# Optimization experiments

Measured on AMD Instinct MI355X. Metric: run time of the kernel, lower is better.

The kernel has to match this reference:

```python
import jax, jax.numpy as jnp
import numpy as np

B, SRC_SEQ, SRC_DIMS = 1024, 336, 64
ORDER, TAR_SEQ = 168, 96


def setup_inputs() -> dict:
    key = jax.random.key(0)
    k1, k2 = jax.random.split(key, 2)
    inputs = jax.random.normal(k1, (B, SRC_SEQ, SRC_DIMS), dtype=jnp.float32)
    # Per-channel Dense(order -> tar_seq_len): stacked kernels and biases.
    W = jax.random.normal(k2, (SRC_DIMS, ORDER, TAR_SEQ), dtype=jnp.float32) * (1.0 / np.sqrt(ORDER))
    b = jnp.zeros((SRC_DIMS, TAR_SEQ), dtype=jnp.float32)
    return {"inputs": inputs, "W": W, "b": b, "training": 0}


def reference(inputs, W, b, training):
    # inputs: [B, S, C]; W: [C, order, T]; b: [C, T]
    order = W.shape[1]
    x = jnp.transpose(inputs, (0, 2, 1))[:, :, -order:]  # [B, C, order]
    # Fused per-channel linear projection (batched over channels):
    y = jnp.einsum('bco,cot->bct', x, W) + b             # [B, C, T]
    return jnp.transpose(y, (0, 2, 1))                    # [B, T, C]
```

## Files before the change

kernel.cpp:

```cpp
#include <hip/hip_runtime.h>

#define BATCH 1024
#define SEQ   336
#define CCH   64
#define ORD   168
#define TT    96
#define OFF   168
#define KP    192
#define RSC   25
#define YSTR  12

typedef __attribute__((ext_vector_type(8))) short  short8;
typedef __attribute__((ext_vector_type(8))) unsigned short ushort8;
typedef __attribute__((ext_vector_type(4))) float  floatx4;

#define WT2_ELEMS ((size_t)CCH * 36 * 512)
#define WS_NEED   (WT2_ELEMS * 2)
#define K2_LDS    (8 * 32 * RSC * 16)

__device__ __forceinline__ unsigned short f2bf(float f) {
    union { float f; unsigned u; } v; v.f = f;
    unsigned r = v.u + 0x7FFF + ((v.u >> 16) & 1);
    return (unsigned short)(r >> 16);
}

__global__ __launch_bounds__(256)
void k1w(const float* __restrict__ W, unsigned short* __restrict__ Wt2)
{
    const int tid = threadIdx.x, l = tid & 63, w = tid >> 6;
    const int wid = blockIdx.x * 4 + w;
    const int kc = wid % 6;
    const int n  = (wid / 6) % 6;
    const int c  = wid / 36;
    const int m  = l & 15, kg = l >> 4;
    const int t  = n * 16 + m;
    ushort8 u;
    #pragma unroll
    for (int j = 0; j < 8; ++j) {
        int o = kc * 32 + kg * 8 + j;
        float val = (o < ORD) ? W[((size_t)c * ORD + o) * TT + t] : 0.f;
        u[j] = f2bf(val);
    }
    *(ushort8*)(Wt2 + (size_t)wid * 512 + l * 8) = u;
}

__global__ __launch_bounds__(512, 2)
void k2f(const float* __restrict__ inp, const unsigned short* __restrict__ Wt2,
         const float* __restrict__ bias, float* __restrict__ out)
{
    extern __shared__ float smem_f[];
    unsigned short* Xs = (unsigned short*)smem_f;

    const int tid = threadIdx.x, l = tid & 63, wv = tid >> 6;
    const int m = l & 15, kg = l >> 4;
    const int btile = (blockIdx.x & 7) | ((blockIdx.x >> 6) << 3);
    const int cg    = (blockIdx.x >> 3) & 7;
    const int b0 = btile * 32, c0 = cg * 8;

    #pragma unroll
    for (int i = 0; i < 3; ++i) {
        int v = tid + i * 512;
        int cq = v & 1, b = (v >> 1) & 31, kchunk = v >> 6;
        floatx4 f[8];
        #pragma unroll
        for (int j = 0; j < 8; ++j) {
            int o = kchunk * 8 + j;
            floatx4 z = {0.f, 0.f, 0.f, 0.f};
            f[j] = (o < ORD)
                ? *(const floatx4*)(inp + ((size_t)(b0 + b) * SEQ + OFF + o) * CCH + c0 + cq * 4)
                : z;
        }
        #pragma unroll
        for (int cc = 0; cc < 4; ++cc) {
            int c = cq * 4 + cc;
            ushort8 u;
            #pragma unroll
            for (int j = 0; j < 8; ++j) u[j] = f2bf(f[j][cc]);
            *(ushort8*)(Xs + (((c * 32 + b) * RSC + (kchunk ^ (c & 7))) << 3)) = u;
        }
    }

    float bv[6];
    #pragma unroll
    for (int n = 0; n < 6; ++n)
        bv[n] = bias[(c0 + wv) * TT + n * 16 + m];

    __syncthreads();

    floatx4 acc0[6] = {}, acc1[6] = {};
    {
        const unsigned short* Wc = Wt2 + (size_t)(c0 + wv) * 36 * 512;
        #pragma unroll
        for (int kc = 0; kc < 6; ++kc) {
            int chunk = (kc * 4 + kg) ^ (wv & 7);
            short8 a0 = *(const short8*)(Xs + (((wv * 32 + m)      * RSC + chunk) << 3));
            short8 a1 = *(const short8*)(Xs + (((wv * 32 + 16 + m) * RSC + chunk) << 3));
            #pragma unroll
            for (int n = 0; n < 6; ++n) {
                short8 bfrag = *(const short8*)(Wc + (size_t)(n * 6 + kc) * 512 + l * 8);
                acc0[n] = __builtin_amdgcn_mfma_f32_16x16x32_bf16(a0, bfrag, acc0[n], 0, 0, 0);
                acc1[n] = __builtin_amdgcn_mfma_f32_16x16x32_bf16(a1, bfrag, acc1[n], 0, 0, 0);
            }
        }
    }

    __syncthreads();

    float* Ys = smem_f;
    #pragma unroll
    for (int rnd = 0; rnd < 2; ++rnd) {
        {
            #pragma unroll
            for (int n = 0; n < 6; ++n)
                #pragma unroll
                for (int r = 0; r < 4; ++r) {
                    int row = kg * 4 + r;
                    float val = (rnd == 0 ? acc0[n][r] : acc1[n][r]) + bv[n];
                    Ys[(row * TT + n * 16 + m) * YSTR + wv] = val;
                }
        }
        __syncthreads();
        {
            int c4  = tid & 1;
            int te  = (tid >> 1) & 15;
            int row = tid >> 5;
            #pragma unroll
            for (int s = 0; s < 6; ++s) {
                int tt = te + s * 16;
                floatx4 y = *(const floatx4*)(Ys + (row * TT + tt) * YSTR + c4 * 4);
                *(floatx4*)(out + ((size_t)(b0 + rnd * 16 + row) * TT + tt) * CCH + c0 + c4 * 4) = y;
            }
        }
        __syncthreads();
    }
}

#define MB  8
#define NT  16
#define KO  8
#define NCH (ORD/KO)
#define WSTRIDE 132
typedef __attribute__((address_space(3))) void* lds_ptr_t;
typedef const __attribute__((address_space(1))) void* gbl_ptr_t;

__global__ __launch_bounds__(256, 4)
void tcl_fallback(const float* __restrict__ inp, const float* __restrict__ W,
                  const float* __restrict__ bias, float* __restrict__ out)
{
    __shared__ float Xsf[MB * KO * CCH];
    __shared__ float Wsf[CCH * WSTRIDE];
    const int tid = threadIdx.x;
    const int c   = tid & 63;
    const int tg  = tid >> 6;
    const int bblk = blockIdx.x & 127;
    const int tblk = blockIdx.x >> 7;
    const int b0 = bblk * MB;
    const int t0 = tblk * NT;
    float acc[MB][4];
    #pragma unroll
    for (int bi = 0; bi < MB; ++bi)
        #pragma unroll
        for (int tj = 0; tj < 4; ++tj) acc[bi][tj] = 0.f;
    for (int ch = 0; ch < NCH; ++ch) {
        const int ob = ch * KO;
        #pragma unroll
        for (int k = 0; k < 4; ++k) {
            int v = tid + k * 256;
            int row = v >> 4, c4 = v & 15;
            int bi = row >> 3, oi = row & 7;
            const float* gp = inp + ((size_t)(b0 + bi) * SEQ + (OFF + ob + oi)) * CCH + c4 * 4;
            __builtin_amdgcn_global_load_lds((gbl_ptr_t)gp, (lds_ptr_t)(Xsf + v * 4), 16, 0, 0);
        }
        float4 wbuf[8];
        #pragma unroll
        for (int k = 0; k < 8; ++k) {
            int v = tid + k * 256;
            int cch = v >> 5, oi = (v >> 2) & 7, t4 = v & 3;
            wbuf[k] = *(const float4*)(W + (size_t)cch * (ORD * TT) + (size_t)(ob + oi) * TT + t0 + t4 * 4);
        }
        #pragma unroll
        for (int k = 0; k < 8; ++k) {
            int v = tid + k * 256;
            int cch = v >> 5, oi = (v >> 2) & 7, t4 = v & 3;
            *(float4*)(Wsf + cch * WSTRIDE + oi * NT + t4 * 4) = wbuf[k];
        }
        __syncthreads();
        #pragma unroll
        for (int oi = 0; oi < KO; ++oi) {
            const float4 wvv = *(const float4*)(Wsf + c * WSTRIDE + oi * NT + tg * 4);
            float xv[MB];
            #pragma unroll
            for (int bi = 0; bi < MB; ++bi) xv[bi] = Xsf[(bi * KO + oi) * CCH + c];
            #pragma unroll
            for (int bi = 0; bi < MB; ++bi) {
                acc[bi][0] += xv[bi] * wvv.x;
                acc[bi][1] += xv[bi] * wvv.y;
                acc[bi][2] += xv[bi] * wvv.z;
                acc[bi][3] += xv[bi] * wvv.w;
            }
        }
        __syncthreads();
    }
    const float4 bvv = *(const float4*)(bias + c * TT + t0 + tg * 4);
    #pragma unroll
    for (int bi = 0; bi < MB; ++bi) {
        size_t base = ((size_t)(b0 + bi) * TT + (t0 + tg * 4)) * CCH + c;
        out[base]           = acc[bi][0] + bvv.x;
        out[base + CCH]     = acc[bi][1] + bvv.y;
        out[base + 2 * CCH] = acc[bi][2] + bvv.z;
        out[base + 3 * CCH] = acc[bi][3] + bvv.w;
    }
}

extern "C" void kernel_launch(void* const* d_in, const int* in_sizes, int n_in,
                              void* d_out, int out_size, void* d_ws, size_t ws_size,
                              hipStream_t stream) {
    const float* inp  = (const float*)d_in[0];
    const float* W    = (const float*)d_in[1];
    const float* bias = (const float*)d_in[2];
    float* out = (float*)d_out;

    if (ws_size >= WS_NEED) {
        unsigned short* Wt2 = (unsigned short*)d_ws;
        k1w<<<576, 256, 0, stream>>>(W, Wt2);
        k2f<<<256, 512, K2_LDS, stream>>>(inp, Wt2, bias, out);
    } else {
        tcl_fallback<<<768, 256, 0, stream>>>(inp, W, bias, out);
    }
}
```

Before: 147.3 us.

## Switch to 32x32x16 MFMA with register-resident weights and smaller channel tiles

Rewrites the main GEMM kernel to use 32x32x16 bf16 MFMA instead of 16x16x32. Each wave now preloads its channel's full weight fragments (36 short8) into registers, and the weight-packing layout changes to match. Blocks shrink to 256 threads covering 4 channels x 32 batches, and the grid doubles to 512 blocks. This cuts LDS weight traffic and instruction count and gives more blocks, but raises register pressure and makes the output store only 16 bytes wide per row.

Result: slower. 157.3 us (+6.8%).

```diff
diff --git a/kernel.cpp b/kernel.cpp
--- a/kernel.cpp
+++ b/kernel.cpp
@@ -7,16 +7,14 @@
 #define TT    96
 #define OFF   168
 #define KP    192
-#define RSC   25
-#define YSTR  12
-
-typedef __attribute__((ext_vector_type(8))) short  short8;
-typedef __attribute__((ext_vector_type(8))) unsigned short ushort8;
-typedef __attribute__((ext_vector_type(4))) float  floatx4;
-
-#define WT2_ELEMS ((size_t)CCH * 36 * 512)
-#define WS_NEED   (WT2_ELEMS * 2)
-#define K2_LDS    (8 * 32 * RSC * 16)
+
+typedef __attribute__((ext_vector_type(8)))  short  short8;
+typedef __attribute__((ext_vector_type(8)))  unsigned short ushort8;
+typedef __attribute__((ext_vector_type(4)))  float  floatx4;
+typedef __attribute__((ext_vector_type(16))) float  floatx16;
+
+#define WT3_ELEMS ((size_t)CCH * 36 * 512)
+#define WS_NEED   (WT3_ELEMS * 2)
 
 __device__ __forceinline__ unsigned short f2bf(float f) {
     union { float f; unsigned u; } v; v.f = f;
@@ -25,113 +23,105 @@
 }
 
 __global__ __launch_bounds__(256)
-void k1w(const float* __restrict__ W, unsigned short* __restrict__ Wt2)
+void k1w(const float* __restrict__ W, unsigned short* __restrict__ Wt3)
 {
     const int tid = threadIdx.x, l = tid & 63, w = tid >> 6;
     const int wid = blockIdx.x * 4 + w;
-    const int kc = wid % 6;
-    const int n  = (wid / 6) % 6;
+    const int kt = wid % 12;
+    const int n  = (wid / 12) % 3;
     const int c  = wid / 36;
-    const int m  = l & 15, kg = l >> 4;
-    const int t  = n * 16 + m;
+    const int tm = l & 31, kh = l >> 5;
+    const int t  = n * 32 + tm;
     ushort8 u;
     #pragma unroll
     for (int j = 0; j < 8; ++j) {
-        int o = kc * 32 + kg * 8 + j;
+        int o = kt * 16 + kh * 8 + j;
         float val = (o < ORD) ? W[((size_t)c * ORD + o) * TT + t] : 0.f;
         u[j] = f2bf(val);
     }
-    *(ushort8*)(Wt2 + (size_t)wid * 512 + l * 8) = u;
-}
-
-__global__ __launch_bounds__(512, 2)
-void k2f(const float* __restrict__ inp, const unsigned short* __restrict__ Wt2,
+    *(ushort8*)(Wt3 + (size_t)wid * 512 + l * 8) = u;
+}
+
+__global__ __launch_bounds__(256, 2)
+void k2g(const float* __restrict__ inp, const unsigned short* __restrict__ Wt3,
          const float* __restrict__ bias, float* __restrict__ out)
 {
-    extern __shared__ float smem_f[];
-    unsigned short* Xs = (unsigned short*)smem_f;
+    __shared__ unsigned short XsU[4 * 12 * 64 * 8];
 
     const int tid = threadIdx.x, l = tid & 63, wv = tid >> 6;
-    const int m = l & 15, kg = l >> 4;
-    const int btile = (blockIdx.x & 7) | ((blockIdx.x >> 6) << 3);
-    const int cg    = (blockIdx.x >> 3) & 7;
-    const int b0 = btile * 32, c0 = cg * 8;
-
-    #pragma unroll
-    for (int i = 0; i < 3; ++i) {
-        int v = tid + i * 512;
-        int cq = v & 1, b = (v >> 1) & 31, kchunk = v >> 6;
+    const int tm = l & 31;
+    const int btile = (blockIdx.x & 7) | ((blockIdx.x >> 7) << 3);
+    const int cg    = (blockIdx.x >> 3) & 15;
+    const int b0 = btile * 32, c0 = cg * 4;
+
+    const unsigned short* Wc = Wt3 + (size_t)(c0 + wv) * 36 * 512 + l * 8;
+    short8 bfr[36];
+    #pragma unroll
+    for (int q = 0; q < 36; ++q)
+        bfr[q] = *(const short8*)(Wc + (size_t)q * 512);
+
+    float bv[3];
+    #pragma unroll
+    for (int n = 0; n < 3; ++n)
+        bv[n] = bias[(c0 + wv) * TT + n * 32 + tm];
+
+    #pragma unroll
+    for (int r = 0; r < 3; ++r) {
+        int v = tid + r * 256;
+        int b = v & 31, kchunk = v >> 5;
+        int kt = kchunk >> 1, kh = kchunk & 1;
         floatx4 f[8];
         #pragma unroll
         for (int j = 0; j < 8; ++j) {
             int o = kchunk * 8 + j;
             floatx4 z = {0.f, 0.f, 0.f, 0.f};
             f[j] = (o < ORD)
-                ? *(const floatx4*)(inp + ((size_t)(b0 + b) * SEQ + OFF + o) * CCH + c0 + cq * 4)
+                ? *(const floatx4*)(inp + ((size_t)(b0 + b) * SEQ + OFF + o) * CCH + c0)
                 : z;
         }
         #pragma unroll
-        for (int cc = 0; cc < 4; ++cc) {
-            int c = cq * 4 + cc;
+        for (int c = 0; c < 4; ++c) {
             ushort8 u;
             #pragma unroll
-            for (int j = 0; j < 8; ++j) u[j] = f2bf(f[j][cc]);
-            *(ushort8*)(Xs + (((c * 32 + b) * RSC + (kchunk ^ (c & 7))) << 3)) = u;
-        }
-    }
-
-    float bv[6];
-    #pragma unroll
-    for (int n = 0; n < 6; ++n)
-        bv[n] = bias[(c0 + wv) * TT + n * 16 + m];
-
+            for (int j = 0; j < 8; ++j) u[j] = f2bf(f[j][c]);
+            *(ushort8*)(XsU + (size_t)(((c * 12 + kt) * 64 + kh * 32 + b)) * 8) = u;
+        }
+    }
     __syncthreads();
 
-    floatx4 acc0[6] = {}, acc1[6] = {};
+    floatx16 acc[3] = {};
     {
-        const unsigned short* Wc = Wt2 + (size_t)(c0 + wv) * 36 * 512;
-        #pragma unroll
-        for (int kc = 0; kc < 6; ++kc) {
-            int chunk = (kc * 4 + kg) ^ (wv & 7);
-            short8 a0 = *(const short8*)(Xs + (((wv * 32 + m)      * RSC + chunk) << 3));
-            short8 a1 = *(const short8*)(Xs + (((wv * 32 + 16 + m) * RSC + chunk) << 3));
-            #pragma unroll
-            for (int n = 0; n < 6; ++n) {
-                short8 bfrag = *(const short8*)(Wc + (size_t)(n * 6 + kc) * 512 + l * 8);
-                acc0[n] = __builtin_amdgcn_mfma_f32_16x16x32_bf16(a0, bfrag, acc0[n], 0, 0, 0);
-                acc1[n] = __builtin_amdgcn_mfma_f32_16x16x32_bf16(a1, bfrag, acc1[n], 0, 0, 0);
+        const unsigned short* Xc = XsU + (size_t)(wv * 12) * 512 + l * 8;
+        #pragma unroll
+        for (int kt = 0; kt < 12; ++kt) {
+            short8 a = *(const short8*)(Xc + kt * 512);
+            acc[0] = __builtin_amdgcn_mfma_f32_32x32x16_bf16(a, bfr[0 * 12 + kt], acc[0], 0, 0, 0);
+            acc[1] = __builtin_amdgcn_mfma_f32_32x32x16_bf16(a, bfr[1 * 12 + kt], acc[1], 0, 0, 0);
+            acc[2] = __builtin_amdgcn_mfma_f32_32x32x16_bf16(a, bfr[2 * 12 + kt], acc[2], 0, 0, 0);
+        }
+    }
+    __syncthreads();
+
+    float* Ys = (float*)XsU;
+    {
+        const int kh = l >> 5;
+        #pragma unroll
+        for (int n = 0; n < 3; ++n)
+            #pragma unroll
+            for (int rg = 0; rg < 16; ++rg) {
+                int b = (rg & 3) + 8 * (rg >> 2) + 4 * kh;
+                Ys[(b * 4 + wv) * TT + n * 32 + tm] = acc[n][rg] + bv[n];
             }
-        }
-    }
-
+    }
     __syncthreads();
 
-    float* Ys = smem_f;
-    #pragma unroll
-    for (int rnd = 0; rnd < 2; ++rnd) {
-        {
-            #pragma unroll
-            for (int n = 0; n < 6; ++n)
-                #pragma unroll
-                for (int r = 0; r < 4; ++r) {
-                    int row = kg * 4 + r;
-                    float val = (rnd == 0 ? acc0[n][r] : acc1[n][r]) + bv[n];
-                    Ys[(row * TT + n * 16 + m) * YSTR + wv] = val;
-                }
-        }
-        __syncthreads();
-        {
-            int c4  = tid & 1;
-            int te  = (tid >> 1) & 15;
-            int row = tid >> 5;
-            #pragma unroll
-            for (int s = 0; s < 6; ++s) {
-                int tt = te + s * 16;
-                floatx4 y = *(const floatx4*)(Ys + (row * TT + tt) * YSTR + c4 * 4);
-                *(floatx4*)(out + ((size_t)(b0 + rnd * 16 + row) * TT + tt) * CCH + c0 + c4 * 4) = y;
-            }
-        }
-        __syncthreads();
+    #pragma unroll
+    for (int r = 0; r < 12; ++r) {
+        int v = tid + r * 256;
+        int b = v / TT, t = v % TT;
+        floatx4 y = { Ys[(b * 4 + 0) * TT + t], Ys[(b * 4 + 1) * TT + t],
+                      Ys[(b * 4 + 2) * TT + t], Ys[(b * 4 + 3) * TT + t] };
+        *(floatx4*)(out + ((size_t)(b0 + b) * TT + t) * CCH + c0) = y;
     }
 }
 
@@ -221,9 +211,9 @@
     float* out = (float*)d_out;
 
     if (ws_size >= WS_NEED) {
-        unsigned short* Wt2 = (unsigned short*)d_ws;
-        k1w<<<576, 256, 0, stream>>>(W, Wt2);
-        k2f<<<256, 512, K2_LDS, stream>>>(inp, Wt2, bias, out);
+        unsigned short* Wt3 = (unsigned short*)d_ws;
+        k1w<<<576, 256, 0, stream>>>(W, Wt3);
+        k2g<<<512, 256, 0, stream>>>(inp, Wt3, bias, out);
     } else {
         tcl_fallback<<<768, 256, 0, stream>>>(inp, W, bias, out);
     }
```
